# Performance work log

Measured on AMD Instinct MI355X. Metric: run time of the kernel, lower is better.

## Reference

```python
import jax, jax.numpy as jnp
import numpy as np

D = 512      # model dim
NH = 8       # heads
DH = 64      # dim per head
M = 256      # num landmarks
ITERS = 6    # pinv iterations
EPS = 1e-5   # layernorm eps


def layer_norm(x, g, b):
    mu = x.mean(-1, keepdims=True)
    var = ((x - mu) ** 2).mean(-1, keepdims=True)
    return (x - mu) * jax.lax.rsqrt(var + EPS) * g + b


def moore_penrose_pinv(x, iters=ITERS):
    abs_x = jnp.abs(x)
    col = abs_x.sum(-1)
    row = abs_x.sum(-2)
    z = jnp.swapaxes(x, -1, -2) / (jnp.max(col) * jnp.max(row))
    I = jnp.eye(x.shape[-1], dtype=x.dtype)
    for _ in range(iters):
        xz = x @ z
        z = 0.25 * z @ (13 * I - xz @ (15 * I - xz @ (7 * I - xz)))
    return z


def nystrom_attention(x, w_qkv, w_out, b_out, res_w):
    B, n0, _ = x.shape
    pad = (M - n0 % M) % M
    x = jnp.pad(x, ((0, 0), (pad, 0), (0, 0)))  # pad at front, like lucidrains
    n = n0 + pad
    qkv = x @ w_qkv  # (B, n, 3*D), no bias
    q, k, v = jnp.split(qkv, 3, axis=-1)
    rs = lambda t: t.reshape(B, n, NH, DH).transpose(0, 2, 1, 3)  # (B,H,n,d)
    q = rs(q) * (DH ** -0.5)
    k = rs(k)
    v = rs(v)
    l = n // M
    q_l = q.reshape(B, NH, M, l, DH).mean(3)  # (B,H,M,d) landmark means
    k_l = k.reshape(B, NH, M, l, DH).mean(3)
    s1 = jnp.einsum('bhnd,bhmd->bhnm', q, k_l)
    s2 = jnp.einsum('bhmd,bhld->bhml', q_l, k_l)
    s3 = jnp.einsum('bhmd,bhnd->bhmn', q_l, k)
    a1 = jax.nn.softmax(s1, -1)
    a2 = jax.nn.softmax(s2, -1)
    a3 = jax.nn.softmax(s3, -1)
    out = a1 @ (moore_penrose_pinv(a2) @ (a3 @ v))  # (B,H,n,d)
    # depthwise residual conv over sequence: Conv2d(heads, heads, (33,1), groups=heads)
    res = jax.lax.conv_general_dilated(v, res_w, (1, 1), 'SAME',
                                       feature_group_count=NH,
                                       dimension_numbers=('NCHW', 'OIHW', 'NCHW'))
    out = out + res
    out = out.transpose(0, 2, 1, 3).reshape(B, n, NH * DH) @ w_out + b_out
    return out[:, -n0:]


def dwconv(x, w, b):
    y = jax.lax.conv_general_dilated(x, w, (1, 1), 'SAME',
                                     feature_group_count=x.shape[1],
                                     dimension_numbers=('NCHW', 'OIHW', 'NCHW'))
    return y + b[None, :, None, None]


def ppeg(x, pw7, pb7, pw5, pb5, pw3, pb3, Hh, Ww):
    cls, feat = x[:, :1], x[:, 1:]
    B, _, C = x.shape
    cnn = feat.transpose(0, 2, 1).reshape(B, C, Hh, Ww)
    y = cnn + dwconv(cnn, pw7, pb7) + dwconv(cnn, pw5, pb5) + dwconv(cnn, pw3, pb3)
    y = y.reshape(B, C, Hh * Ww).transpose(0, 2, 1)
    return jnp.concatenate([cls, y], axis=1)


def _forward(x, w_fc1, b_fc1, cls_token, ln1_g, ln1_b, qkv1_w, out1_w, out1_b, res1_w,
             ln2_g, ln2_b, qkv2_w, out2_w, out2_b, res2_w,
             pw7, pb7, pw5, pb5, pw3, pb3, lnf_g, lnf_b, w_fc2, b_fc2):
    h = jax.nn.relu(x @ w_fc1 + b_fc1)  # (B, N, 512)
    Hn = h.shape[1]
    s = int(np.ceil(np.sqrt(Hn)))  # static grid side
    add = s * s - Hn
    h = jnp.concatenate([h, h[:, :add]], axis=1)
    B = h.shape[0]
    cls = jnp.broadcast_to(cls_token, (B, 1, D))
    h = jnp.concatenate([cls, h], axis=1)
    h = h + nystrom_attention(layer_norm(h, ln1_g, ln1_b), qkv1_w, out1_w, out1_b, res1_w)
    h = ppeg(h, pw7, pb7, pw5, pb5, pw3, pb3, s, s)
    h = h + nystrom_attention(layer_norm(h, ln2_g, ln2_b), qkv2_w, out2_w, out2_b, res2_w)
    h = layer_norm(h, lnf_g, lnf_b)[:, 0]
    return h @ w_fc2 + b_fc2


def setup_inputs() -> dict:
    key = jax.random.key(0)
    ks = jax.random.split(key, 16)
    g = lambda k, shp, s=0.02: jax.random.normal(k, shp, dtype=jnp.float32) * s
    z = lambda n: jnp.zeros((n,), jnp.float32)
    o = lambda n: jnp.ones((n,), jnp.float32)
    B, N, DIN, NC = 2, 10000, 1024, 2
    return {
        'x': jax.random.normal(ks[0], (B, N, DIN), dtype=jnp.float32),
        'w_fc1': g(ks[1], (DIN, D)), 'b_fc1': z(D),
        'cls_token': g(ks[2], (1, 1, D), 1.0),
        'ln1_g': o(D), 'ln1_b': z(D),
        'qkv1_w': g(ks[3], (D, 3 * D)),
        'out1_w': g(ks[4], (D, D)), 'out1_b': z(D),
        'res1_w': g(ks[5], (NH, 1, 33, 1)),
        'ln2_g': o(D), 'ln2_b': z(D),
        'qkv2_w': g(ks[6], (D, 3 * D)),
        'out2_w': g(ks[7], (D, D)), 'out2_b': z(D),
        'res2_w': g(ks[8], (NH, 1, 33, 1)),
        'pw7': g(ks[9], (D, 1, 7, 7)), 'pb7': z(D),
        'pw5': g(ks[10], (D, 1, 5, 5)), 'pb5': z(D),
        'pw3': g(ks[11], (D, 1, 3, 3)), 'pb3': z(D),
        'lnf_g': o(D), 'lnf_b': z(D),
        'w_fc2': g(ks[12], (D, NC)), 'b_fc2': z(NC),
    }


def reference(x, w_fc1, b_fc1, cls_token, ln1_g, ln1_b, qkv1_w, out1_w, out1_b, res1_w,
              ln2_g, ln2_b, qkv2_w, out2_w, out2_b, res2_w,
              pw7, pb7, pw5, pb5, pw3, pb3, lnf_g, lnf_b, w_fc2, b_fc2):
    logits = _forward(x, w_fc1, b_fc1, cls_token, ln1_g, ln1_b, qkv1_w, out1_w, out1_b, res1_w,
                      ln2_g, ln2_b, qkv2_w, out2_w, out2_b, res2_w,
                      pw7, pb7, pw5, pb5, pw3, pb3, lnf_g, lnf_b, w_fc2, b_fc2)
    Y_prob = jax.nn.softmax(logits, -1)
    Y_hat = jnp.argmax(logits, -1)
    return logits, Y_prob, Y_hat
```

## Files before the change

### kernel.cpp

```cpp
#include <hip/hip_runtime.h>
#include <math.h>

#define FLAG_RELU 1
#define FLAG_BIAS 2
#define FLAG_ACC  4
#define FLAG_ATOMIC 8

static constexpr int BB   = 2;
static constexpr int N0   = 10000;
static constexpr int DIN  = 1024;
static constexpr int D    = 512;
static constexpr int NH   = 8;
static constexpr int DH   = 64;
static constexpr int MM   = 256;
static constexpr int SEQ  = 10240;
static constexpr int PADR = 239;
static constexpr int NTOK = 10001;
static constexpr int LL   = 40;
static constexpr float EPS_ = 1e-5f;

typedef short short8v __attribute__((ext_vector_type(8)));
typedef float f32x4 __attribute__((ext_vector_type(4)));

__device__ __forceinline__ void atomicMaxPosF(float* addr, float v) {
    atomicMax((unsigned int*)addr, __float_as_uint(v));
}
__device__ __forceinline__ ushort f2bf(float f) {
    unsigned u = __float_as_uint(f);
    return (ushort)((u + 0x7FFFu + ((u >> 16) & 1u)) >> 16);
}
__device__ __forceinline__ float bf2f(ushort h) {
    return __uint_as_float(((unsigned)h) << 16);
}
__device__ __forceinline__ void split4(float4 f, ushort* ph, ushort* pl) {
    ushort4 hv, lv;
    hv.x = f2bf(f.x); lv.x = f2bf(f.x - bf2f(hv.x));
    hv.y = f2bf(f.y); lv.y = f2bf(f.y - bf2f(hv.y));
    hv.z = f2bf(f.z); lv.z = f2bf(f.z - bf2f(hv.z));
    hv.w = f2bf(f.w); lv.w = f2bf(f.w - bf2f(hv.w));
    *(ushort4*)ph = hv; *(ushort4*)pl = lv;
}
__device__ __forceinline__ void split8r(const float* p, short8v& h, short8v& l) {
    ushort hb[8], lb[8];
    split4(*(const float4*)p,     &hb[0], &lb[0]);
    split4(*(const float4*)(p+4), &hb[4], &lb[4]);
    h = *(short8v*)hb; l = *(short8v*)lb;
}

__global__ __launch_bounds__(256)
void mgemm128(const float* __restrict__ A, int lda, long long sAz,
              const ushort* __restrict__ BtH, const ushort* __restrict__ BtL, int ldbt,
              float* __restrict__ C, int ldc, long long sCz, const float* __restrict__ bias,
              int M, int N, int K, int flags, int qcols, float qscale)
{
    __shared__ ushort AsH[4*128*8], AsL[4*128*8], BsH[4*128*8], BsL[4*128*8];
    A += (size_t)blockIdx.z * sAz;
    C += (size_t)blockIdx.z * sCz;
    int t = threadIdx.x;
    int m0 = blockIdx.y * 128, n0 = blockIdx.x * 128;
    int w = t >> 6, lane = t & 63, q = lane >> 4, r = lane & 15;
    int wm = w >> 1, wn = w & 1;
    f32x4 acc[4][4];
    #pragma unroll
    for (int i = 0; i < 4; i++)
        #pragma unroll
        for (int j = 0; j < 4; j++) acc[i][j] = (f32x4){0.f,0.f,0.f,0.f};

    int srow = t >> 1, scg = (t & 1) * 16;
    int qg = (t & 1) * 2;
    int gm = m0 + srow;
    float4 pa0, pa1, pa2, pa3;
    uint4  pb0, pb1, pb2, pb3;
    {
        pa0 = pa1 = pa2 = pa3 = make_float4(0,0,0,0);
        if (gm < M) {
            const float* ap = A + (size_t)gm * lda + scg;
            pa0 = *(const float4*)(ap);   pa1 = *(const float4*)(ap+4);
            pa2 = *(const float4*)(ap+8); pa3 = *(const float4*)(ap+12);
        }
        size_t gb = (size_t)(n0 + srow) * ldbt + scg;
        pb0 = *(const uint4*)(BtH + gb); pb1 = *(const uint4*)(BtH + gb + 8);
        pb2 = *(const uint4*)(BtL + gb); pb3 = *(const uint4*)(BtL + gb + 8);
    }
    for (int k0 = 0; k0 < K; k0 += 32) {
        {
            ushort hb[16], lb[16];
            split4(pa0, &hb[0],  &lb[0]);
            split4(pa1, &hb[4],  &lb[4]);
            split4(pa2, &hb[8],  &lb[8]);
            split4(pa3, &hb[12], &lb[12]);
            *(uint4*)&AsH[(qg  )*1024 + srow*8] = *(uint4*)&hb[0];
            *(uint4*)&AsH[(qg+1)*1024 + srow*8] = *(uint4*)&hb[8];
            *(uint4*)&AsL[(qg  )*1024 + srow*8] = *(uint4*)&lb[0];
            *(uint4*)&AsL[(qg+1)*1024 + srow*8] = *(uint4*)&lb[8];
            *(uint4*)&BsH[(qg  )*1024 + srow*8] = pb0;
            *(uint4*)&BsH[(qg+1)*1024 + srow*8] = pb1;
            *(uint4*)&BsL[(qg  )*1024 + srow*8] = pb2;
            *(uint4*)&BsL[(qg+1)*1024 + srow*8] = pb3;
        }
        __syncthreads();
        if (k0 + 32 < K) {
            pa0 = pa1 = pa2 = pa3 = make_float4(0,0,0,0);
            if (gm < M) {
                const float* ap = A + (size_t)gm * lda + k0 + 32 + scg;
                pa0 = *(const float4*)(ap);   pa1 = *(const float4*)(ap+4);
                pa2 = *(const float4*)(ap+8); pa3 = *(const float4*)(ap+12);
            }
            size_t gb = (size_t)(n0 + srow) * ldbt + k0 + 32 + scg;
            pb0 = *(const uint4*)(BtH + gb); pb1 = *(const uint4*)(BtH + gb + 8);
            pb2 = *(const uint4*)(BtL + gb); pb3 = *(const uint4*)(BtL + gb + 8);
        }
        short8v ah[4], al[4];
        #pragma unroll
        for (int mi = 0; mi < 4; mi++) {
            int row = wm*64 + mi*16 + r;
            ah[mi] = *(const short8v*)&AsH[q*1024 + row*8];
            al[mi] = *(const short8v*)&AsL[q*1024 + row*8];
        }
        #pragma unroll
        for (int ni = 0; ni < 4; ni++) {
            int col = wn*64 + ni*16 + r;
            short8v bh = *(const short8v*)&BsH[q*1024 + col*8];
            short8v bl = *(const short8v*)&BsL[q*1024 + col*8];
            #pragma unroll
            for (int mi = 0; mi < 4; mi++) {
                acc[mi][ni] = __builtin_amdgcn_mfma_f32_16x16x32_bf16(ah[mi], bh, acc[mi][ni], 0,0,0);
                acc[mi][ni] = __builtin_amdgcn_mfma_f32_16x16x32_bf16(ah[mi], bl, acc[mi][ni], 0,0,0);
                acc[mi][ni] = __builtin_amdgcn_mfma_f32_16x16x32_bf16(al[mi], bh, acc[mi][ni], 0,0,0);
            }
        }
        __syncthreads();
    }
    #pragma unroll
    for (int mi = 0; mi < 4; mi++)
        #pragma unroll
        for (int ni = 0; ni < 4; ni++) {
            int gcol = n0 + wn*64 + ni*16 + r;
            float qs = (gcol < qcols) ? qscale : 1.f;
            float bv = (flags & FLAG_BIAS) ? bias[gcol] : 0.f;
            #pragma unroll
            for (int rg = 0; rg < 4; rg++) {
                int grow = m0 + wm*64 + mi*16 + q*4 + rg;
                if (grow >= M) continue;
                float v = acc[mi][ni][rg] * qs + bv;
                if (flags & FLAG_RELU) v = fmaxf(v, 0.f);
                float* cp = C + (size_t)grow * ldc + gcol;
                if (flags & FLAG_ACC) v += *cp;
                *cp = v;
            }
        }
}

__global__ __launch_bounds__(256)
void mbgemm64(const float* __restrict__ Abase, long long sAb, long long sAh, long long sAz, int lda,
              const ushort* __restrict__ BtH, const ushort* __restrict__ BtL,
              const float* __restrict__ Bnt, long long sBb, long long sBh, int ldb,
              float* __restrict__ Cbase, long long sCb, long long sCh, long long sCz, int ldc,
              ushort* __restrict__ eTH, ushort* __restrict__ eTL, long long sT, int ldct,
              int M, int N, int K, int nchunk,
              float dg, float bsc, float osc, int slab0, int flags)
{
    __shared__ ushort AsH[4*64*8], AsL[4*64*8], BsH[4*64*8], BsL[4*64*8];
    int zi = blockIdx.z / nchunk, ch = blockIdx.z % nchunk;
    int g = slab0 + zi, b = g >> 3, h = g & 7;
    const float* A = Abase + (size_t)b*sAb + (size_t)h*sAh + (size_t)zi*sAz;
    float* C = Cbase ? (Cbase + (size_t)b*sCb + (size_t)h*sCh + (size_t)zi*sCz) : nullptr;
    int kpc = K / nchunk;
    int kb = ch * kpc, ke = kb + kpc;
    int t = threadIdx.x;
    int m0 = blockIdx.y * 64, n0 = blockIdx.x * 64;
    int w = t >> 6, lane = t & 63, q = lane >> 4, r = lane & 15;
    int wm = w >> 1, wn = w & 1;
    f32x4 acc[2][2];
    #pragma unroll
    for (int i = 0; i < 2; i++)
        #pragma unroll
        for (int j = 0; j < 2; j++) acc[i][j] = (f32x4){0.f,0.f,0.f,0.f};

    int srow = t >> 2, scg = (t & 3) * 8;
    int qg = t & 3;
    const float* Abp = Bnt ? (Bnt + (size_t)b*sBb + (size_t)h*sBh) : nullptr;
    float4 pa0, pa1;
    float4 pf0, pf1;
    uint4  pu0, pu1;
    {
        const float* ap = A + (size_t)(m0 + srow) * lda + kb + scg;
        pa0 = *(const float4*)ap; pa1 = *(const float4*)(ap+4);
        if (Bnt) {
            const float* bp = Abp + (size_t)(n0 + srow) * ldb + kb + scg;
            pf0 = *(const float4*)bp; pf1 = *(const float4*)(bp+4);
        } else {
            size_t gb = (size_t)b*sBb + (size_t)h*sBh + (size_t)(n0 + srow) * ldb + kb + scg;
            pu0 = *(const uint4*)(BtH + gb); pu1 = *(const uint4*)(BtL + gb);
        }
    }
    for (int k0 = kb; k0 < ke; k0 += 32) {
        {
            ushort hb[8], lb[8];
            split4(pa0, &hb[0], &lb[0]);
            split4(pa1, &hb[4], &lb[4]);
            *(uint4*)&AsH[qg*512 + srow*8] = *(uint4*)&hb[0];
            *(uint4*)&AsL[qg*512 + srow*8] = *(uint4*)&lb[0];
            if (Bnt) {
                ushort hc[8], lc[8];
                split4(pf0, &hc[0], &lc[0]);
                split4(pf1, &hc[4], &lc[4]);
                *(uint4*)&BsH[qg*512 + srow*8] = *(uint4*)&hc[0];
                *(uint4*)&BsL[qg*512 + srow*8] = *(uint4*)&lc[0];
            } else {
                *(uint4*)&BsH[qg*512 + srow*8] = pu0;
                *(uint4*)&BsL[qg*512 + srow*8] = pu1;
            }
        }
        __syncthreads();
        if (k0 + 32 < ke) {
            const float* ap = A + (size_t)(m0 + srow) * lda + k0 + 32 + scg;
            pa0 = *(const float4*)ap; pa1 = *(const float4*)(ap+4);
            if (Bnt) {
                const float* bp = Abp + (size_t)(n0 + srow) * ldb + k0 + 32 + scg;
                pf0 = *(const float4*)bp; pf1 = *(const float4*)(bp+4);
            } else {
                size_t gb = (size_t)b*sBb + (size_t)h*sBh + (size_t)(n0 + srow) * ldb + k0 + 32 + scg;
                pu0 = *(const uint4*)(BtH + gb); pu1 = *(const uint4*)(BtL + gb);
            }
        }
        short8v ah[2], al[2];
        #pragma unroll
        for (int mi = 0; mi < 2; mi++) {
            int row = wm*32 + mi*16 + r;
            ah[mi] = *(const short8v*)&AsH[q*512 + row*8];
            al[mi] = *(const short8v*)&AsL[q*512 + row*8];
        }
        #pragma unroll
        for (int ni = 0; ni < 2; ni++) {
            int col = wn*32 + ni*16 + r;
            short8v bh = *(const short8v*)&BsH[q*512 + col*8];
            short8v bl = *(const short8v*)&BsL[q*512 + col*8];
            #pragma unroll
            for (int mi = 0; mi < 2; mi++) {
                acc[mi][ni] = __builtin_amdgcn_mfma_f32_16x16x32_bf16(ah[mi], bh, acc[mi][ni], 0,0,0);
                acc[mi][ni] = __builtin_amdgcn_mfma_f32_16x16x32_bf16(ah[mi], bl, acc[mi][ni], 0,0,0);
                acc[mi][ni] = __builtin_amdgcn_mfma_f32_16x16x32_bf16(al[mi], bh, acc[mi][ni], 0,0,0);
            }
        }
        __syncthreads();
    }
    bool dgnz = (dg != 0.f);
    #pragma unroll
    for (int mi = 0; mi < 2; mi++)
        #pragma unroll
        for (int ni = 0; ni < 2; ni++) {
            int gm0 = m0 + wm*32 + mi*16 + q*4;
            int gn  = n0 + wn*32 + ni*16 + r;
            float v[4];
            #pragma unroll
            for (int rg = 0; rg < 4; rg++) {
                float u = bsc * acc[mi][ni][rg];
                if (dgnz) u += dg * A[(size_t)(gm0+rg) * lda + gn];
                v[rg] = osc * u;
            }
            if (C) {
                if (flags & FLAG_ATOMIC) {
                    #pragma unroll
                    for (int rg = 0; rg < 4; rg++)
                        atomicAdd(C + (size_t)(gm0+rg) * ldc + gn, v[rg]);
                } else {
                    #pragma unroll
                    for (int rg = 0; rg < 4; rg++)
                        C[(size_t)(gm0+rg) * ldc + gn] = v[rg];
                }
            }
            if (eTH) {
                ushort4 hv, lv;
                hv.x = f2bf(v[0]); lv.x = f2bf(v[0] - bf2f(hv.x));
                hv.y = f2bf(v[1]); lv.y = f2bf(v[1] - bf2f(hv.y));
                hv.z = f2bf(v[2]); lv.z = f2bf(v[2] - bf2f(hv.z));
                hv.w = f2bf(v[3]); lv.w = f2bf(v[3] - bf2f(hv.w));
                size_t to = (size_t)g * sT + (size_t)gn * ldct + gm0;
                *(ushort4*)(eTH + to) = hv;
                *(ushort4*)(eTL + to) = lv;
            }
        }
}

__global__ __launch_bounds__(256)
void a1_fused(const float* __restrict__ qkv,
              const ushort* __restrict__ klH, const ushort* __restrict__ klL,
              const ushort* __restrict__ wbH, const ushort* __restrict__ wbL,
              float* __restrict__ attn)
{
    __shared__ float Pc[256*66];
    __shared__ float redm[4][64];
    __shared__ float reds[4][64];
    int g = blockIdx.y, b = g >> 3, h = g & 7;
    int tok0 = blockIdx.x * 64;
    int t = threadIdx.x;
    int w = t >> 6, lane = t & 63, q = lane >> 4, r = lane & 15;

    f32x4 acc[4][4];
    #pragma unroll
    for (int i = 0; i < 4; i++)
        #pragma unroll
        for (int j = 0; j < 4; j++) acc[i][j] = (f32x4){0.f,0.f,0.f,0.f};
    #pragma unroll
    for (int k0 = 0; k0 < 64; k0 += 32) {
        short8v ah[4], al[4];
        #pragma unroll
        for (int mi = 0; mi < 4; mi++) {
            const float* ap = qkv + ((size_t)b*SEQ + tok0 + mi*16 + r) * 1536
                            + h*DH + k0 + q*8;
            split8r(ap, ah[mi], al[mi]);
        }
        #pragma unroll
        for (int ni = 0; ni < 4; ni++) {
            size_t kb = ((size_t)g*MM + w*64 + ni*16 + r) * DH + k0 + q*8;
            short8v bh = *(const short8v*)(klH + kb);
            short8v bl = *(const short8v*)(klL + kb);
            #pragma unroll
            for (int mi = 0; mi < 4; mi++) {
                acc[mi][ni] = __builtin_amdgcn_mfma_f32_16x16x32_bf16(ah[mi], bh, acc[mi][ni], 0,0,0);
                acc[mi][ni] = __builtin_amdgcn_mfma_f32_16x16x32_bf16(ah[mi], bl, acc[mi][ni], 0,0,0);
                acc[mi][ni] = __builtin_amdgcn_mfma_f32_16x16x32_bf16(al[mi], bh, acc[mi][ni], 0,0,0);
            }
        }
    }
    #pragma unroll
    for (int mi = 0; mi < 4; mi++)
        #pragma unroll
        for (int rg = 0; rg < 4; rg++) {
            float m = fmaxf(fmaxf(acc[mi][0][rg], acc[mi][1][rg]),
                            fmaxf(acc[mi][2][rg], acc[mi][3][rg]));
            for (int o = 8; o > 0; o >>= 1) m = fmaxf(m, __shfl_xor(m, o));
            if (r == 0) redm[w][mi*16 + q*4 + rg] = m;
        }
    __syncthreads();
    #pragma unroll
    for (int mi = 0; mi < 4; mi++)
        #pragma unroll
        for (int rg = 0; rg < 4; rg++) {
            int row = mi*16 + q*4 + rg;
            float gm = fmaxf(fmaxf(redm[0][row], redm[1][row]),
                             fmaxf(redm[2][row], redm[3][row]));
            float s = 0.f;
            #pragma unroll
            for (int ni = 0; ni < 4; ni++) {
                float e = expf(acc[mi][ni][rg] - gm);
                acc[mi][ni][rg] = e;
                s += e;
            }
            for (int o = 8; o > 0; o >>= 1) s += __shfl_xor(s, o);
            if (r == 0) reds[w][row] = s;
        }
    #pragma unroll
    for (int mi = 0; mi < 4; mi++)
        #pragma unroll
        for (int ni = 0; ni < 4; ni++) {
            int col = w*64 + ni*16 + r;
            int row0 = mi*16 + q*4;
            float* pp = &Pc[col*66 + row0];
            *(float2*)(pp)     = make_float2(acc[mi][ni][0], acc[mi][ni][1]);
            *(float2*)(pp + 2) = make_float2(acc[mi][ni][2], acc[mi][ni][3]);
        }
    __syncthreads();
    f32x4 oacc[4];
    #pragma unroll
    for (int ni = 0; ni < 4; ni++) oacc[ni] = (f32x4){0.f,0.f,0.f,0.f};
    for (int k0 = 0; k0 < 8; k0++) {
        short8v ph, pl;
        {
            ushort hb[8], lb[8];
            #pragma unroll
            for (int j = 0; j < 8; j++) {
                int k = k0*32 + q*8 + j;
                float p = Pc[k*66 + w*16 + r];
                hb[j] = f2bf(p); lb[j] = f2bf(p - bf2f(hb[j]));
            }
            ph = *(short8v*)hb; pl = *(short8v*)lb;
        }
        #pragma unroll
        for (int ni = 0; ni < 4; ni++) {
            size_t wo = ((size_t)g*64 + ni*16 + r) * MM + k0*32 + q*8;
            short8v bh = *(const short8v*)(wbH + wo);
            short8v bl = *(const short8v*)(wbL + wo);
            oacc[ni] = __builtin_amdgcn_mfma_f32_16x16x32_bf16(ph, bh, oacc[ni], 0,0,0);
            oacc[ni] = __builtin_amdgcn_mfma_f32_16x16x32_bf16(ph, bl, oacc[ni], 0,0,0);
            oacc[ni] = __builtin_amdgcn_mfma_f32_16x16x32_bf16(pl, bh, oacc[ni], 0,0,0);
        }
    }
    float inv[4];
    #pragma unroll
    for (int rg = 0; rg < 4; rg++) {
        int row = w*16 + q*4 + rg;
        inv[rg] = 1.0f / (reds[0][row] + reds[1][row] + reds[2][row] + reds[3][row]);
    }
    #pragma unroll
    for (int ni = 0; ni < 4; ni++)
        #pragma unroll
        for (int rg = 0; rg < 4; rg++) {
            int tok = tok0 + w*16 + q*4 + rg;
            attn[((size_t)b*SEQ + tok) * D + h*DH + ni*16 + r] = oacc[ni][rg] * inv[rg];
        }
}

__global__ __launch_bounds__(256)
void convsplitT(const float* __restrict__ in, ushort* __restrict__ oh, ushort* __restrict__ ol,
                int R, int C, int ldin, long long sInB, long long sInH, long long sInZ,
                int ldo, long long sOutZ)
{
    __shared__ float tile[32][33];
    int z = blockIdx.z, b = z >> 3, h = z & 7;
    const float* I = in + (size_t)b*sInB + (size_t)h*sInH + (size_t)z*sInZ;
    int p0 = blockIdx.x * 32, c0 = blockIdx.y * 32;
    int tx = threadIdx.x & 31, ty = threadIdx.x >> 5;
    #pragma unroll
    for (int k = 0; k < 4; k++) {
        int rr = p0 + ty + k*8, cc = c0 + tx;
        tile[ty + k*8][tx] = (rr < R && cc < C) ? I[(size_t)rr * ldin + cc] : 0.f;
    }
    __syncthreads();
    #pragma unroll
    for (int k = 0; k < 4; k++) {
        int rr = p0 + tx, cc = c0 + ty + k*8;
        if (rr < R && cc < C) {
            float f = tile[tx][ty + k*8];
            ushort hv = f2bf(f);
            size_t o = (size_t)z * sOutZ + (size_t)cc * ldo + rr;
            oh[o] = hv; ol[o] = f2bf(f - bf2f(hv));
        }
    }
}

__global__ void fill_cls(const float* __restrict__ cls, float* __restrict__ H) {
    H[(size_t)blockIdx.x * NTOK * D + threadIdx.x] = cls[threadIdx.x];
}

__global__ __launch_bounds__(256)
void ln_pad(const float* __restrict__ H, const float* __restrict__ g,
            const float* __restrict__ bt, float* __restrict__ out)
{
    int blk = blockIdx.x;
    int b = blk / SEQ, i = blk % SEQ;
    int t = threadIdx.x;
    float* orow = out + (size_t)blk * D;
    if (i < PADR) { orow[t] = 0.f; orow[t+256] = 0.f; return; }
    const float* x = H + ((size_t)b * NTOK + (i - PADR)) * D;
    float v0 = x[t], v1 = x[t+256];
    __shared__ float w1[4], w2[4];
    float s = v0 + v1;
    for (int o = 32; o > 0; o >>= 1) s += __shfl_xor(s, o);
    if ((t & 63) == 0) w1[t >> 6] = s;
    __syncthreads();
    float mu = (w1[0]+w1[1]+w1[2]+w1[3]) * (1.0f / D);
    float d0 = v0 - mu, d1 = v1 - mu;
    float qq = d0*d0 + d1*d1;
    for (int o = 32; o > 0; o >>= 1) qq += __shfl_xor(qq, o);
    if ((t & 63) == 0) w2[t >> 6] = qq;
    __syncthreads();
    float rs = rsqrtf((w2[0]+w2[1]+w2[2]+w2[3]) * (1.0f / D) + EPS_);
    orow[t]     = d0 * rs * g[t]     + bt[t];
    orow[t+256] = d1 * rs * g[t+256] + bt[t+256];
}

__global__ __launch_bounds__(512)
void landmarks(const float* __restrict__ qkv, float* __restrict__ ql,
               float* __restrict__ klt, ushort* __restrict__ klH, ushort* __restrict__ klL)
{
    int blk = blockIdx.x;
    int b = blk >> 8, m = blk & 255;
    int c = threadIdx.x;
    const float* base = qkv + ((size_t)b * SEQ + (size_t)m * LL) * 1536;
    float sq0=0,sq1=0,sq2=0,sq3=0, sk0=0,sk1=0,sk2=0,sk3=0;
    for (int tt = 0; tt < LL; tt += 4) {
        const float* rr = base + (size_t)tt * 1536;
        sq0 += rr[c];          sk0 += rr[512 + c];
        sq1 += rr[1536 + c];   sk1 += rr[1536 + 512 + c];
        sq2 += rr[3072 + c];   sk2 += rr[3072 + 512 + c];
        sq3 += rr[4608 + c];   sk3 += rr[4608 + 512 + c];
    }
    float sq = (sq0+sq1+sq2+sq3) * (1.0f / LL);
    float sk = (sk0+sk1+sk2+sk3) * (1.0f / LL);
    int h = c >> 6, d = c & 63;
    int slab = b * NH + h;
    ql [((size_t)slab * MM + m) * DH + d] = sq;
    klt[((size_t)slab * DH + d) * MM + m] = sk;
    size_t kidx = ((size_t)slab * MM + m) * DH + d;
    ushort kh = f2bf(sk);
    klH[kidx] = kh; klL[kidx] = f2bf(sk - bf2f(kh));
}

__global__ __launch_bounds__(256)
void s2_softmax(const float* __restrict__ ql, const float* __restrict__ klt,
                float* __restrict__ a2)
{
    int blk = blockIdx.x;
    int m = blk & 255, slab = blk >> 8;
    int j = threadIdx.x;
    __shared__ float q[64];
    __shared__ float red[256];
    if (j < 64) q[j] = ql[((size_t)slab * MM + m) * DH + j];
    __syncthreads();
    const float* kt = klt + (size_t)slab * DH * MM;
    float s = 0.f;
    #pragma unroll 8
    for (int kk = 0; kk < 64; kk++) s = fmaf(q[kk], kt[kk*MM + j], s);
    red[j] = s; __syncthreads();
    for (int o = 128; o > 0; o >>= 1) { if (j < o) red[j] = fmaxf(red[j], red[j+o]); __syncthreads(); }
    float mx = red[0]; __syncthreads();
    float e = expf(s - mx);
    red[j] = e; __syncthreads();
    for (int o = 128; o > 0; o >>= 1) { if (j < o) red[j] += red[j+o]; __syncthreads(); }
    a2[((size_t)slab * MM + m) * MM + j] = e / red[0];
}

__global__ void zero_scr(float* s) { if (threadIdx.x < 2) s[threadIdx.x] = 0.f; }

__global__ __launch_bounds__(256)
void a2_alpha(const float* __restrict__ a2, float* __restrict__ scr)
{
    int slab = blockIdx.x, t = threadIdx.x;
    const float* A = a2 + (size_t)slab * MM * MM;
    float cs = 0.f, rs = 0.f;
    for (int rr = 0; rr < MM; rr++) cs += fabsf(A[(size_t)rr * MM + t]);
    for (int cc = 0; cc < MM; cc++) rs += fabsf(A[(size_t)t * MM + cc]);
    __shared__ float red[256];
    red[t] = rs; __syncthreads();
    for (int o = 128; o > 0; o >>= 1) { if (t < o) red[t] = fmaxf(red[t], red[t+o]); __syncthreads(); }
    float mrs = red[0]; __syncthreads();
    red[t] = cs; __syncthreads();
    for (int o = 128; o > 0; o >>= 1) { if (t < o) red[t] = fmaxf(red[t], red[t+o]); __syncthreads(); }
    float mcs = red[0];
    if (t == 0) { atomicMaxPosF(scr + 0, mrs); atomicMaxPosF(scr + 1, mcs); }
}

__global__ __launch_bounds__(256)
void z_init(const float* __restrict__ a2, const float* __restrict__ scr,
            float* __restrict__ z, ushort* __restrict__ zTh, ushort* __restrict__ zTl)
{
    size_t idx = (size_t)blockIdx.x * 256 + threadIdx.x;
    int slab = (int)(idx >> 16), rr = (int)((idx >> 8) & 255), cc = (int)(idx & 255);
    float inv = 1.0f / (scr[0] * scr[1]);
    z[idx] = a2[((size_t)slab << 16) + (size_t)cc * MM + rr] * inv;
    float tv = a2[idx] * inv;
    ushort th = f2bf(tv);
    zTh[idx] = th; zTl[idx] = f2bf(tv - bf2f(th));
}

__global__ __launch_bounds__(256)
void s3_softmax(float* __restrict__ s3)
{
    float* row = s3 + (size_t)blockIdx.x * SEQ;
    int t = threadIdx.x;
    float4 v[10];
    #pragma unroll
    for (int i = 0; i < 10; i++) v[i] = *(const float4*)(row + 4*(i*256 + t));
    float mx = -3.4e38f;
    #pragma unroll
    for (int i = 0; i < 10; i++)
        mx = fmaxf(mx, fmaxf(fmaxf(v[i].x, v[i].y), fmaxf(v[i].z, v[i].w)));
    __shared__ float red[4];
    for (int o = 32; o > 0; o >>= 1) mx = fmaxf(mx, __shfl_xor(mx, o));
    if ((t & 63) == 0) red[t >> 6] = mx;
    __syncthreads();
    mx = fmaxf(fmaxf(red[0], red[1]), fmaxf(red[2], red[3]));
    float sum = 0.f;
    #pragma unroll
    for (int i = 0; i < 10; i++) {
        v[i].x = expf(v[i].x - mx); v[i].y = expf(v[i].y - mx);
        v[i].z = expf(v[i].z - mx); v[i].w = expf(v[i].w - mx);
        sum += v[i].x + v[i].y + v[i].z + v[i].w;
    }
    __shared__ float red2[4];
    for (int o = 32; o > 0; o >>= 1) sum += __shfl_xor(sum, o);
    if ((t & 63) == 0) red2[t >> 6] = sum;
    __syncthreads();
    float inv = 1.0f / (red2[0] + red2[1] + red2[2] + red2[3]);
    #pragma unroll
    for (int i = 0; i < 10; i++) {
        v[i].x *= inv; v[i].y *= inv; v[i].z *= inv; v[i].w *= inv;
        *(float4*)(row + 4*(i*256 + t)) = v[i];
    }
}

__global__ __launch_bounds__(512)
void res_add(const float* __restrict__ qkv, const float* __restrict__ rw,
             float* __restrict__ attn)
{
    int blk = blockIdx.x;
    int b = blk / (SEQ/16), i0 = (blk % (SEQ/16)) * 16;
    int c = threadIdx.x, h = c >> 6;
    __shared__ float w[NH*33];
    if (c < NH*33) w[c] = rw[c];
    __syncthreads();
    float acc[16];
    float* ab = attn + ((size_t)b * SEQ + i0) * D + c;
    #pragma unroll
    for (int rr = 0; rr < 16; rr++) acc[rr] = ab[(size_t)rr * D];
    const float* vb = qkv + (size_t)b * SEQ * 1536 + 2*D + c;
    const float* wh = w + h * 33;
    #pragma unroll 4
    for (int jj = 0; jj < 48; jj++) {
        int j = i0 + jj - 16;
        float val = ((unsigned)j < (unsigned)SEQ) ? vb[(size_t)j * 1536] : 0.f;
        #pragma unroll
        for (int rr = 0; rr < 16; rr++) {
            int ky = jj - rr;
            if (ky >= 0 && ky < 33) acc[rr] = fmaf(val, wh[ky], acc[rr]);
        }
    }
    #pragma unroll
    for (int rr = 0; rr < 16; rr++) ab[(size_t)rr * D] = acc[rr];
}

__global__ __launch_bounds__(256)
void t_fw(const float* __restrict__ H, float* __restrict__ P)
{
    __shared__ float tile[32][33];
    int p0 = blockIdx.x * 32, c0 = blockIdx.y * 32, b = blockIdx.z;
    int tx = threadIdx.x & 31, ty = threadIdx.x >> 5;
    #pragma unroll
    for (int k = 0; k < 4; k++) {
        int pos = p0 + ty + k*8;
        tile[ty + k*8][tx] = (pos < 10000)
            ? H[((size_t)b * NTOK + 1 + pos) * D + c0 + tx] : 0.f;
    }
    __syncthreads();
    #pragma unroll
    for (int k = 0; k < 4; k++) {
        int c = c0 + ty + k*8, pos = p0 + tx;
        if (pos < 10000)
            P[((size_t)b * D + c) * 10000 + pos] = tile[tx][ty + k*8];
    }
}

__global__ __launch_bounds__(256)
void ppeg_conv(const float* __restrict__ P,
               const float* __restrict__ w7, const float* __restrict__ b7,
               const float* __restrict__ w5, const float* __restrict__ b5,
               const float* __restrict__ w3, const float* __restrict__ b3,
               float* __restrict__ Q)
{
    __shared__ float PS[106 * 107];
    __shared__ float w7s[49], w5s[25], w3s[9];
    int blk = blockIdx.x;
    int b = blk >> 9, c = blk & 511;
    int t = threadIdx.x;
    for (int idx = t; idx < 106*107; idx += 256) PS[idx] = 0.f;
    if (t < 49) w7s[t] = w7[(size_t)c * 49 + t];
    if (t < 25) w5s[t] = w5[(size_t)c * 25 + t];
    if (t < 9)  w3s[t] = w3[(size_t)c * 9 + t];
    float bsum = b7[c] + b5[c] + b3[c];
    __syncthreads();
    const float* Pin = P + ((size_t)b * D + c) * 10000;
    for (int p = t; p < 10000; p += 256) {
        int y = p / 100, x = p - y * 100;
        PS[(y + 3) * 107 + x + 3] = Pin[p];
    }
    __syncthreads();
    float* Qo = Q + ((size_t)b * D + c) * 10000;
    for (int task = t; task < 2500; task += 256) {
        int ry = task / 100, x = task - ry * 100;
        int y0 = ry * 4;
        float a0 = bsum + PS[(y0+3)*107 + x+3];
        float a1 = bsum + PS[(y0+4)*107 + x+3];
        float a2 = bsum + PS[(y0+5)*107 + x+3];
        float a3 = bsum + PS[(y0+6)*107 + x+3];
        #pragma unroll
        for (int rr = 0; rr < 10; rr++) {
            const float* rp = &PS[(y0 + rr) * 107 + x];
            #pragma unroll
            for (int kx = 0; kx < 7; kx++) {
                float v = rp[kx];
                if (rr < 7)            a0 = fmaf(v, w7s[rr*7 + kx], a0);
                if (rr >= 1 && rr < 8) a1 = fmaf(v, w7s[(rr-1)*7 + kx], a1);
                if (rr >= 2 && rr < 9) a2 = fmaf(v, w7s[(rr-2)*7 + kx], a2);
                if (rr >= 3)           a3 = fmaf(v, w7s[(rr-3)*7 + kx], a3);
            }
        }
        #pragma unroll
        for (int rr = 0; rr < 8; rr++) {
            const float* rp = &PS[(y0 + rr + 1) * 107 + x + 1];
            #pragma unroll
            for (int kx = 0; kx < 5; kx++) {
                float v = rp[kx];
                if (rr < 5)            a0 = fmaf(v, w5s[rr*5 + kx], a0);
                if (rr >= 1 && rr < 6) a1 = fmaf(v, w5s[(rr-1)*5 + kx], a1);
                if (rr >= 2 && rr < 7) a2 = fmaf(v, w5s[(rr-2)*5 + kx], a2);
                if (rr >= 3)           a3 = fmaf(v, w5s[(rr-3)*5 + kx], a3);
            }
        }
        #pragma unroll
        for (int rr = 0; rr < 6; rr++) {
            const float* rp = &PS[(y0 + rr + 2) * 107 + x + 2];
            #pragma unroll
            for (int kx = 0; kx < 3; kx++) {
                float v = rp[kx];
                if (rr < 3)            a0 = fmaf(v, w3s[rr*3 + kx], a0);
                if (rr >= 1 && rr < 4) a1 = fmaf(v, w3s[(rr-1)*3 + kx], a1);
                if (rr >= 2 && rr < 5) a2 = fmaf(v, w3s[(rr-2)*3 + kx], a2);
                if (rr >= 3)           a3 = fmaf(v, w3s[(rr-3)*3 + kx], a3);
            }
        }
        Qo[(y0+0)*100 + x] = a0;
        Qo[(y0+1)*100 + x] = a1;
        Qo[(y0+2)*100 + x] = a2;
        Qo[(y0+3)*100 + x] = a3;
    }
}

__global__ __launch_bounds__(256)
void t_bw(const float* __restrict__ Q, float* __restrict__ H)
{
    __shared__ float tile[32][33];
    int p0 = blockIdx.x * 32, c0 = blockIdx.y * 32, b = blockIdx.z;
    int tx = threadIdx.x & 31, ty = threadIdx.x >> 5;
    #pragma unroll
    for (int k = 0; k < 4; k++) {
        int c = c0 + ty + k*8, pos = p0 + tx;
        tile[ty + k*8][tx] = (pos < 10000)
            ? Q[((size_t)b * D + c) * 10000 + pos] : 0.f;
    }
    __syncthreads();
    #pragma unroll
    for (int k = 0; k < 4; k++) {
        int pos = p0 + ty + k*8;
        if (pos < 10000)
            H[((size_t)b * NTOK + 1 + pos) * D + c0 + tx] = tile[tx][ty + k*8];
    }
}

__global__ __launch_bounds__(512)
void final_head(const float* __restrict__ H, const float* __restrict__ g,
                const float* __restrict__ bt, const float* __restrict__ w2,
                const float* __restrict__ b2, float* __restrict__ out)
{
    int b = blockIdx.x, t = threadIdx.x;
    __shared__ float red[512];
    float v = H[(size_t)b * NTOK * D + t];
    red[t] = v; __syncthreads();
    for (int o = 256; o > 0; o >>= 1) { if (t < o) red[t] += red[t+o]; __syncthreads(); }
    float mu = red[0] * (1.0f / D); __syncthreads();
    float dv = v - mu;
    red[t] = dv*dv; __syncthreads();
    for (int o = 256; o > 0; o >>= 1) { if (t < o) red[t] += red[t+o]; __syncthreads(); }
    float rstd = rsqrtf(red[0] * (1.0f / D) + EPS_); __syncthreads();
    float xn = dv * rstd * g[t] + bt[t];
    red[t] = xn * w2[2*t]; __syncthreads();
    for (int o = 256; o > 0; o >>= 1) { if (t < o) red[t] += red[t+o]; __syncthreads(); }
    float l0 = red[0] + b2[0]; __syncthreads();
    red[t] = xn * w2[2*t+1]; __syncthreads();
    for (int o = 256; o > 0; o >>= 1) { if (t < o) red[t] += red[t+o]; __syncthreads(); }
    float l1 = red[0] + b2[1];
    if (t == 0) {
        out[b*2+0] = l0; out[b*2+1] = l1;
        float mx = fmaxf(l0, l1);
        float e0 = expf(l0 - mx), e1 = expf(l1 - mx);
        float ssum = e0 + e1;
        out[4 + b*2 + 0] = e0 / ssum;
        out[4 + b*2 + 1] = e1 / ssum;
        out[8 + b] = (l1 > l0) ? 1.0f : 0.0f;
    }
}

extern "C" void kernel_launch(void* const* d_in, const int* in_sizes, int n_in,
                              void* d_out, int out_size, void* d_ws, size_t ws_size,
                              hipStream_t stream)
{
    const float* x      = (const float*)d_in[0];
    const float* w_fc1  = (const float*)d_in[1];
    const float* b_fc1  = (const float*)d_in[2];
    const float* cls    = (const float*)d_in[3];
    const float* ln1_g  = (const float*)d_in[4];
    const float* ln1_b  = (const float*)d_in[5];
    const float* qkv1_w = (const float*)d_in[6];
    const float* out1_w = (const float*)d_in[7];
    const float* out1_b = (const float*)d_in[8];
    const float* res1_w = (const float*)d_in[9];
    const float* ln2_g  = (const float*)d_in[10];
    const float* ln2_b  = (const float*)d_in[11];
    const float* qkv2_w = (const float*)d_in[12];
    const float* out2_w = (const float*)d_in[13];
    const float* out2_b = (const float*)d_in[14];
    const float* res2_w = (const float*)d_in[15];
    const float* pw7 = (const float*)d_in[16];
    const float* pb7 = (const float*)d_in[17];
    const float* pw5 = (const float*)d_in[18];
    const float* pb5 = (const float*)d_in[19];
    const float* pw3 = (const float*)d_in[20];
    const float* pb3 = (const float*)d_in[21];
    const float* lnf_g = (const float*)d_in[22];
    const float* lnf_b = (const float*)d_in[23];
    const float* w_fc2 = (const float*)d_in[24];
    const float* b_fc2 = (const float*)d_in[25];

    float* ws = (float*)d_ws;
    size_t off = 0;
    auto alloc = [&](size_t n) { float* p = ws + off; off += (n + 63) & ~(size_t)63; return p; };
    float* H    = alloc((size_t)BB * NTOK * D);
    float* LN   = alloc((size_t)BB * SEQ * D);
    float* QKV  = alloc((size_t)BB * SEQ * 3 * D);
    float* QL   = alloc((size_t)BB * NH * MM * DH);
    float* KLT  = alloc((size_t)BB * NH * DH * MM);
    float* A2   = alloc((size_t)BB * NH * MM * MM);
    float* ZA   = alloc((size_t)BB * NH * MM * MM);
    float* ZB   = alloc((size_t)BB * NH * MM * MM);
    float* XZ   = alloc((size_t)BB * NH * MM * MM);
    float* A3V  = alloc((size_t)BB * NH * MM * DH);
    float* WB   = alloc((size_t)BB * NH * MM * DH);
    float* S3   = alloc((size_t)8 * MM * SEQ);
    float* SCR  = alloc(64);
    auto ualloc = [&](size_t n) { ushort* p = (ushort*)(ws + off); off += ((n + 127) / 2) & ~(size_t)63; return p; };
    ushort* WTfcH = ualloc((size_t)512 * 1024);
    ushort* WTfcL = ualloc((size_t)512 * 1024);
    ushort* WTqH  = ualloc((size_t)1536 * 512);
    ushort* WTqL  = ualloc((size_t)1536 * 512);
    ushort* WToH  = ualloc((size_t)512 * 512);
    ushort* WToL  = ualloc((size_t)512 * 512);
    ushort* klBH  = ualloc((size_t)16 * MM * DH);
    ushort* klBL  = ualloc((size_t)16 * MM * DH);
    float*  ATTN = LN;
    ushort* VTH  = (ushort*)LN;
    ushort* VTL  = VTH + (size_t)16 * DH * SEQ;
    ushort* A3VTH = (ushort*)ZB;
    ushort* A3VTL = A3VTH + (size_t)16 * DH * MM;
    ushort* WBTH  = A3VTL + (size_t)16 * DH * MM;
    ushort* WBTL  = WBTH  + (size_t)16 * DH * MM;
    ushort* PT   = (ushort*)S3;
    const size_t PS_ = (size_t)16 * 65536;
    ushort* zTAH = PT;            ushort* zTAL = PT + PS_;
    ushort* zTBH = PT + 2*PS_;    ushort* zTBL = PT + 3*PS_;
    ushort* XZTH = PT + 4*PS_;    ushort* XZTL = PT + 5*PS_;
    ushort* T1TH = PT + 6*PS_;    ushort* T1TL = PT + 7*PS_;
    ushort* T2TH = PT + 8*PS_;    ushort* T2TL = PT + 9*PS_;
    (void)ws_size; (void)in_sizes; (void)n_in; (void)out_size;

    convsplitT<<<dim3(32,16,1), 256, 0, stream>>>(w_fc1, WTfcH, WTfcL, 1024, 512, 512, 0,0,0, 1024, 0);
    mgemm128<<<dim3(4, 79, BB), 256, 0, stream>>>(x, DIN, (long long)N0*DIN,
        WTfcH, WTfcL, 1024, H + D, D, (long long)NTOK*D, b_fc1,
        N0, D, DIN, FLAG_BIAS|FLAG_RELU, 0, 1.f);
    fill_cls<<<BB, D, 0, stream>>>(cls, H);

    auto attention = [&](const float* lg, const float* lb,
                         const float* qw, const float* ow,
                         const float* ob, const float* rw)
    {
        convsplitT<<<dim3(16,48,1), 256, 0, stream>>>(qw, WTqH, WTqL, 512, 1536, 1536, 0,0,0, 512, 0);
        convsplitT<<<dim3(16,16,1), 256, 0, stream>>>(ow, WToH, WToL, 512, 512, 512, 0,0,0, 512, 0);
        ln_pad<<<BB*SEQ, 256, 0, stream>>>(H, lg, lb, LN);
        mgemm128<<<dim3(12, 160, 1), 256, 0, stream>>>(LN, D, 0, WTqH, WTqL, D,
            QKV, 3*D, 0, nullptr, BB*SEQ, 3*D, D, 0, D, 0.125f);
        convsplitT<<<dim3(320, 2, 16), 256, 0, stream>>>(QKV + 2*D, VTH, VTL,
            SEQ, DH, 1536, (long long)SEQ*1536, 64, 0, SEQ, (long long)DH*SEQ);
        landmarks<<<BB*MM, 512, 0, stream>>>(QKV, QL, KLT, klBH, klBL);
        s2_softmax<<<BB*NH*MM, 256, 0, stream>>>(QL, KLT, A2);
        zero_scr<<<1, 64, 0, stream>>>(SCR);
        a2_alpha<<<BB*NH, 256, 0, stream>>>(A2, SCR);
        z_init<<<BB*NH*MM*MM/256, 256, 0, stream>>>(A2, SCR, ZA, zTAH, zTAL);
        float* z = ZA; float* zn = ZB;
        ushort *zTcH = zTAH, *zTcL = zTAL, *zTnH = zTBH, *zTnL = zTBL;
        for (int it = 0; it < 6; it++) {
            dim3 g(4, 4, 16);
            mbgemm64<<<g,256,0,stream>>>(A2, 0,0,65536LL, MM,
                zTcH, zTcL, nullptr, 8LL*65536, 65536LL, MM,
                XZ, 0,0,65536LL, MM, XZTH, XZTL, 65536LL, MM,
                MM, MM, MM, 1, 0.f, 1.f, 1.f, 0, 0);
            mbgemm64<<<g,256,0,stream>>>(XZ, 0,0,65536LL, MM,
                XZTH, XZTL, nullptr, 8LL*65536, 65536LL, MM,
                nullptr, 0,0,0, MM, T1TH, T1TL, 65536LL, MM,
                MM, MM, MM, 1, 7.f, -1.f, 1.f, 0, 0);
            mbgemm64<<<g,256,0,stream>>>(XZ, 0,0,65536LL, MM,
                T1TH, T1TL, nullptr, 8LL*65536, 65536LL, MM,
                nullptr, 0,0,0, MM, T2TH, T2TL, 65536LL, MM,
                MM, MM, MM, 1, 15.f, -1.f, 1.f, 0, 0);
            mbgemm64<<<g,256,0,stream>>>(z, 0,0,65536LL, MM,
                T2TH, T2TL, nullptr, 8LL*65536, 65536LL, MM,
                zn, 0,0,65536LL, MM, zTnH, zTnL, 65536LL, MM,
                MM, MM, MM, 1, 13.f, -1.f, 0.25f, 0, 0);
            float* ts = z; z = zn; zn = ts;
            ushort* uh = zTcH; zTcH = zTnH; zTnH = uh;
            ushort* ul = zTcL; zTcL = zTnL; zTnL = ul;
        }
        for (int grp = 0; grp < 2; grp++) {
            int slab0 = grp * 8;
            mbgemm64<<<dim3(160, 4, 8), 256, 0, stream>>>(QL, 8LL*16384, 16384LL, 0, DH,
                nullptr, nullptr, QKV + D, (long long)SEQ*1536, 64LL, 1536,
                S3, 0,0,(long long)MM*SEQ, SEQ, nullptr, nullptr, 0, 0,
                MM, SEQ, DH, 1, 0.f, 1.f, 1.f, slab0, 0);
            s3_softmax<<<8*MM, 256, 0, stream>>>(S3);
            hipMemsetAsync(A3V + (size_t)slab0 * MM * DH, 0,
                           (size_t)8 * MM * DH * sizeof(float), stream);
            mbgemm64<<<dim3(1, 4, 8*16), 256, 0, stream>>>(S3, 0,0,(long long)MM*SEQ, SEQ,
                VTH, VTL, nullptr, 8LL*DH*SEQ, (long long)DH*SEQ, SEQ,
                A3V, 8LL*16384, 16384LL, 0, DH, nullptr, nullptr, 0, 0,
                MM, DH, SEQ, 16, 0.f, 1.f, 1.f, slab0, FLAG_ATOMIC);
        }
        convsplitT<<<dim3(8, 2, 16), 256, 0, stream>>>(A3V, A3VTH, A3VTL,
            MM, DH, DH, 0, 0, 16384LL, MM, 16384LL);
        mbgemm64<<<dim3(1, 4, 16), 256, 0, stream>>>(z, 0,0,65536LL, MM,
            A3VTH, A3VTL, nullptr, 8LL*16384, 16384LL, MM,
            WB, 8LL*16384, 16384LL, 0, DH, WBTH, WBTL, 16384LL, MM,
            MM, DH, MM, 1, 0.f, 1.f, 1.f, 0, 0);
        a1_fused<<<dim3(SEQ/64, 16), 256, 0, stream>>>(QKV, klBH, klBL, WBTH, WBTL, ATTN);
        res_add<<<BB*SEQ/16, 512, 0, stream>>>(QKV, rw, ATTN);
        mgemm128<<<dim3(4, 79, BB), 256, 0, stream>>>(ATTN + (size_t)PADR*D, D, (long long)SEQ*D,
            WToH, WToL, D, H, D, (long long)NTOK*D, ob,
            NTOK, D, D, FLAG_BIAS|FLAG_ACC, 0, 1.f);
    };

    attention(ln1_g, ln1_b, qkv1_w, out1_w, out1_b, res1_w);

    {
        float* Pp = S3;
        float* Qp = S3 + (size_t)BB * D * 10000;
        dim3 tg((10000 + 31)/32, D/32, BB);
        t_fw<<<tg, 256, 0, stream>>>(H, Pp);
        ppeg_conv<<<BB*D, 256, 0, stream>>>(Pp, pw7, pb7, pw5, pb5, pw3, pb3, Qp);
        t_bw<<<tg, 256, 0, stream>>>(Qp, H);
    }

    attention(ln2_g, ln2_b, qkv2_w, out2_w, out2_b, res2_w);

    final_head<<<BB, 512, 0, stream>>>(H, lnf_g, lnf_b, w_fc2, b_fc2, (float*)d_out);
}
```

Before: 2.372 ms.

## Fuse s3 softmax normalization into A3·V GEMM load and shrink a1 tile

The s3 softmax kernel now computes only the per-row max and inverse sum. The exp and normalization are applied inside mbgemm64 when it loads the A operand, which removes a full write of the normalized S3 buffer. Separately, a1_fused drops to 32 tokens per block, doubling the grid and cutting shared-memory use to raise occupancy. In exchange, the GEMM recomputes exp in its load path, and the smaller a1 tile means more reloads of landmark keys and weights.

```diff
diff --git a/kernel.cpp b/kernel.cpp
--- a/kernel.cpp
+++ b/kernel.cpp
@@ -157,6 +157,7 @@
               const float* __restrict__ Bnt, long long sBb, long long sBh, int ldb,
               float* __restrict__ Cbase, long long sCb, long long sCh, long long sCz, int ldc,
               ushort* __restrict__ eTH, ushort* __restrict__ eTL, long long sT, int ldct,
+              const float* __restrict__ rowM, const float* __restrict__ rowI,
               int M, int N, int K, int nchunk,
               float dg, float bsc, float osc, int slab0, int flags)
 {
@@ -179,6 +180,12 @@
 
     int srow = t >> 2, scg = (t & 3) * 8;
     int qg = t & 3;
+    float rmv = 0.f, riv = 1.f;
+    bool doexp = (rowM != nullptr);
+    if (doexp) {
+        rmv = rowM[(size_t)zi * MM + m0 + srow];
+        riv = rowI[(size_t)zi * MM + m0 + srow];
+    }
     const float* Abp = Bnt ? (Bnt + (size_t)b*sBb + (size_t)h*sBh) : nullptr;
     float4 pa0, pa1;
     float4 pf0, pf1;
@@ -196,9 +203,16 @@
     }
     for (int k0 = kb; k0 < ke; k0 += 32) {
         {
+            float4 qa0 = pa0, qa1 = pa1;
+            if (doexp) {
+                qa0.x = expf(qa0.x - rmv) * riv; qa0.y = expf(qa0.y - rmv) * riv;
+                qa0.z = expf(qa0.z - rmv) * riv; qa0.w = expf(qa0.w - rmv) * riv;
+                qa1.x = expf(qa1.x - rmv) * riv; qa1.y = expf(qa1.y - rmv) * riv;
+                qa1.z = expf(qa1.z - rmv) * riv; qa1.w = expf(qa1.w - rmv) * riv;
+            }
             ushort hb[8], lb[8];
-            split4(pa0, &hb[0], &lb[0]);
-            split4(pa1, &hb[4], &lb[4]);
+            split4(qa0, &hb[0], &lb[0]);
+            split4(qa1, &hb[4], &lb[4]);
             *(uint4*)&AsH[qg*512 + srow*8] = *(uint4*)&hb[0];
             *(uint4*)&AsL[qg*512 + srow*8] = *(uint4*)&lb[0];
             if (Bnt) {
@@ -289,24 +303,24 @@
               const ushort* __restrict__ wbH, const ushort* __restrict__ wbL,
               float* __restrict__ attn)
 {
-    __shared__ float Pc[256*66];
-    __shared__ float redm[4][64];
-    __shared__ float reds[4][64];
+    __shared__ float Pc[256*35];
+    __shared__ float redm[4][32];
+    __shared__ float reds[4][32];
     int g = blockIdx.y, b = g >> 3, h = g & 7;
-    int tok0 = blockIdx.x * 64;
+    int tok0 = blockIdx.x * 32;
     int t = threadIdx.x;
     int w = t >> 6, lane = t & 63, q = lane >> 4, r = lane & 15;
 
-    f32x4 acc[4][4];
-    #pragma unroll
-    for (int i = 0; i < 4; i++)
+    f32x4 acc[2][4];
+    #pragma unroll
+    for (int i = 0; i < 2; i++)
         #pragma unroll
         for (int j = 0; j < 4; j++) acc[i][j] = (f32x4){0.f,0.f,0.f,0.f};
     #pragma unroll
     for (int k0 = 0; k0 < 64; k0 += 32) {
-        short8v ah[4], al[4];
-        #pragma unroll
-        for (int mi = 0; mi < 4; mi++) {
+        short8v ah[2], al[2];
+        #pragma unroll
+        for (int mi = 0; mi < 2; mi++) {
             const float* ap = qkv + ((size_t)b*SEQ + tok0 + mi*16 + r) * 1536
                             + h*DH + k0 + q*8;
             split8r(ap, ah[mi], al[mi]);
@@ -317,7 +331,7 @@
             short8v bh = *(const short8v*)(klH + kb);
             short8v bl = *(const short8v*)(klL + kb);
             #pragma unroll
-            for (int mi = 0; mi < 4; mi++) {
+            for (int mi = 0; mi < 2; mi++) {
                 acc[mi][ni] = __builtin_amdgcn_mfma_f32_16x16x32_bf16(ah[mi], bh, acc[mi][ni], 0,0,0);
                 acc[mi][ni] = __builtin_amdgcn_mfma_f32_16x16x32_bf16(ah[mi], bl, acc[mi][ni], 0,0,0);
                 acc[mi][ni] = __builtin_amdgcn_mfma_f32_16x16x32_bf16(al[mi], bh, acc[mi][ni], 0,0,0);
@@ -325,7 +339,7 @@
         }
     }
     #pragma unroll
-    for (int mi = 0; mi < 4; mi++)
+    for (int mi = 0; mi < 2; mi++)
         #pragma unroll
         for (int rg = 0; rg < 4; rg++) {
             float m = fmaxf(fmaxf(acc[mi][0][rg], acc[mi][1][rg]),
@@ -335,7 +349,7 @@
         }
     __syncthreads();
     #pragma unroll
-    for (int mi = 0; mi < 4; mi++)
+    for (int mi = 0; mi < 2; mi++)
         #pragma unroll
         for (int rg = 0; rg < 4; rg++) {
             int row = mi*16 + q*4 + rg;
@@ -352,19 +366,20 @@
             if (r == 0) reds[w][row] = s;
         }
     #pragma unroll
-    for (int mi = 0; mi < 4; mi++)
+    for (int mi = 0; mi < 2; mi++)
         #pragma unroll
         for (int ni = 0; ni < 4; ni++) {
             int col = w*64 + ni*16 + r;
             int row0 = mi*16 + q*4;
-            float* pp = &Pc[col*66 + row0];
+            float* pp = &Pc[col*35 + row0];
             *(float2*)(pp)     = make_float2(acc[mi][ni][0], acc[mi][ni][1]);
             *(float2*)(pp + 2) = make_float2(acc[mi][ni][2], acc[mi][ni][3]);
         }
     __syncthreads();
-    f32x4 oacc[4];
-    #pragma unroll
-    for (int ni = 0; ni < 4; ni++) oacc[ni] = (f32x4){0.f,0.f,0.f,0.f};
+    int wm = w & 1, wn = w >> 1;
+    f32x4 oacc[2];
+    #pragma unroll
+    for (int ni = 0; ni < 2; ni++) oacc[ni] = (f32x4){0.f,0.f,0.f,0.f};
     for (int k0 = 0; k0 < 8; k0++) {
         short8v ph, pl;
         {
@@ -372,14 +387,14 @@
             #pragma unroll
             for (int j = 0; j < 8; j++) {
                 int k = k0*32 + q*8 + j;
-                float p = Pc[k*66 + w*16 + r];
+                float p = Pc[k*35 + wm*16 + r];
                 hb[j] = f2bf(p); lb[j] = f2bf(p - bf2f(hb[j]));
             }
             ph = *(short8v*)hb; pl = *(short8v*)lb;
         }
         #pragma unroll
-        for (int ni = 0; ni < 4; ni++) {
-            size_t wo = ((size_t)g*64 + ni*16 + r) * MM + k0*32 + q*8;
+        for (int ni = 0; ni < 2; ni++) {
+            size_t wo = ((size_t)g*64 + wn*32 + ni*16 + r) * MM + k0*32 + q*8;
             short8v bh = *(const short8v*)(wbH + wo);
             short8v bl = *(const short8v*)(wbL + wo);
             oacc[ni] = __builtin_amdgcn_mfma_f32_16x16x32_bf16(ph, bh, oacc[ni], 0,0,0);
@@ -390,15 +405,15 @@
     float inv[4];
     #pragma unroll
     for (int rg = 0; rg < 4; rg++) {
-        int row = w*16 + q*4 + rg;
+        int row = wm*16 + q*4 + rg;
         inv[rg] = 1.0f / (reds[0][row] + reds[1][row] + reds[2][row] + reds[3][row]);
     }
     #pragma unroll
-    for (int ni = 0; ni < 4; ni++)
+    for (int ni = 0; ni < 2; ni++)
         #pragma unroll
         for (int rg = 0; rg < 4; rg++) {
-            int tok = tok0 + w*16 + q*4 + rg;
-            attn[((size_t)b*SEQ + tok) * D + h*DH + ni*16 + r] = oacc[ni][rg] * inv[rg];
+            int tok = tok0 + wm*16 + q*4 + rg;
+            attn[((size_t)b*SEQ + tok) * D + h*DH + wn*32 + ni*16 + r] = oacc[ni][rg] * inv[rg];
         }
 }
 
@@ -546,9 +561,10 @@
 }
 
 __global__ __launch_bounds__(256)
-void s3_softmax(float* __restrict__ s3)
-{
-    float* row = s3 + (size_t)blockIdx.x * SEQ;
+void s3_maxsum(const float* __restrict__ s3, float* __restrict__ rowM,
+               float* __restrict__ rowI)
+{
+    const float* row = s3 + (size_t)blockIdx.x * SEQ;
     int t = threadIdx.x;
     float4 v[10];
     #pragma unroll
@@ -565,19 +581,16 @@
     float sum = 0.f;
     #pragma unroll
     for (int i = 0; i < 10; i++) {
-        v[i].x = expf(v[i].x - mx); v[i].y = expf(v[i].y - mx);
-        v[i].z = expf(v[i].z - mx); v[i].w = expf(v[i].w - mx);
-        sum += v[i].x + v[i].y + v[i].z + v[i].w;
+        sum += expf(v[i].x - mx) + expf(v[i].y - mx)
+             + expf(v[i].z - mx) + expf(v[i].w - mx);
     }
     __shared__ float red2[4];
     for (int o = 32; o > 0; o >>= 1) sum += __shfl_xor(sum, o);
     if ((t & 63) == 0) red2[t >> 6] = sum;
     __syncthreads();
-    float inv = 1.0f / (red2[0] + red2[1] + red2[2] + red2[3]);
-    #pragma unroll
-    for (int i = 0; i < 10; i++) {
-        v[i].x *= inv; v[i].y *= inv; v[i].z *= inv; v[i].w *= inv;
-        *(float4*)(row + 4*(i*256 + t)) = v[i];
+    if (t == 0) {
+        rowM[blockIdx.x] = mx;
+        rowI[blockIdx.x] = 1.0f / (red2[0] + red2[1] + red2[2] + red2[3]);
     }
 }
 
@@ -808,6 +821,8 @@
     float* WB   = alloc((size_t)BB * NH * MM * DH);
     float* S3   = alloc((size_t)8 * MM * SEQ);
     float* SCR  = alloc(64);
+    float* ROWM = alloc((size_t)8 * MM);
+    float* ROWI = alloc((size_t)8 * MM);
     auto ualloc = [&](size_t n) { ushort* p = (ushort*)(ws + off); off += ((n + 127) / 2) & ~(size_t)63; return p; };
     ushort* WTfcH = ualloc((size_t)512 * 1024);
     ushort* WTfcL = ualloc((size_t)512 * 1024);
@@ -862,18 +877,22 @@
             mbgemm64<<<g,256,0,stream>>>(A2, 0,0,65536LL, MM,
                 zTcH, zTcL, nullptr, 8LL*65536, 65536LL, MM,
                 XZ, 0,0,65536LL, MM, XZTH, XZTL, 65536LL, MM,
+                nullptr, nullptr,
                 MM, MM, MM, 1, 0.f, 1.f, 1.f, 0, 0);
             mbgemm64<<<g,256,0,stream>>>(XZ, 0,0,65536LL, MM,
                 XZTH, XZTL, nullptr, 8LL*65536, 65536LL, MM,
                 nullptr, 0,0,0, MM, T1TH, T1TL, 65536LL, MM,
+                nullptr, nullptr,
                 MM, MM, MM, 1, 7.f, -1.f, 1.f, 0, 0);
             mbgemm64<<<g,256,0,stream>>>(XZ, 0,0,65536LL, MM,
                 T1TH, T1TL, nullptr, 8LL*65536, 65536LL, MM,
                 nullptr, 0,0,0, MM, T2TH, T2TL, 65536LL, MM,
+                nullptr, nullptr,
                 MM, MM, MM, 1, 15.f, -1.f, 1.f, 0, 0);
             mbgemm64<<<g,256,0,stream>>>(z, 0,0,65536LL, MM,
                 T2TH, T2TL, nullptr, 8LL*65536, 65536LL, MM,
                 zn, 0,0,65536LL, MM, zTnH, zTnL, 65536LL, MM,
+                nullptr, nullptr,
                 MM, MM, MM, 1, 13.f, -1.f, 0.25f, 0, 0);
             float* ts = z; z = zn; zn = ts;
             ushort* uh = zTcH; zTcH = zTnH; zTnH = uh;
@@ -884,13 +903,15 @@
             mbgemm64<<<dim3(160, 4, 8), 256, 0, stream>>>(QL, 8LL*16384, 16384LL, 0, DH,
                 nullptr, nullptr, QKV + D, (long long)SEQ*1536, 64LL, 1536,
                 S3, 0,0,(long long)MM*SEQ, SEQ, nullptr, nullptr, 0, 0,
+                nullptr, nullptr,
                 MM, SEQ, DH, 1, 0.f, 1.f, 1.f, slab0, 0);
-            s3_softmax<<<8*MM, 256, 0, stream>>>(S3);
+            s3_maxsum<<<8*MM, 256, 0, stream>>>(S3, ROWM, ROWI);
             hipMemsetAsync(A3V + (size_t)slab0 * MM * DH, 0,
                            (size_t)8 * MM * DH * sizeof(float), stream);
             mbgemm64<<<dim3(1, 4, 8*16), 256, 0, stream>>>(S3, 0,0,(long long)MM*SEQ, SEQ,
                 VTH, VTL, nullptr, 8LL*DH*SEQ, (long long)DH*SEQ, SEQ,
                 A3V, 8LL*16384, 16384LL, 0, DH, nullptr, nullptr, 0, 0,
+                ROWM, ROWI,
                 MM, DH, SEQ, 16, 0.f, 1.f, 1.f, slab0, FLAG_ATOMIC);
         }
         convsplitT<<<dim3(8, 2, 16), 256, 0, stream>>>(A3V, A3VTH, A3VTL,
@@ -898,8 +919,9 @@
         mbgemm64<<<dim3(1, 4, 16), 256, 0, stream>>>(z, 0,0,65536LL, MM,
             A3VTH, A3VTL, nullptr, 8LL*16384, 16384LL, MM,
             WB, 8LL*16384, 16384LL, 0, DH, WBTH, WBTL, 16384LL, MM,
+            nullptr, nullptr,
             MM, DH, MM, 1, 0.f, 1.f, 1.f, 0, 0);
-        a1_fused<<<dim3(SEQ/64, 16), 256, 0, stream>>>(QKV, klBH, klBL, WBTH, WBTL, ATTN);
+        a1_fused<<<dim3(SEQ/32, 16), 256, 0, stream>>>(QKV, klBH, klBL, WBTH, WBTL, ATTN);
         res_add<<<BB*SEQ/16, 512, 0, stream>>>(QKV, rw, ATTN);
         mgemm128<<<dim3(4, 79, BB), 256, 0, stream>>>(ATTN + (size_t)PADR*D, D, (long long)SEQ*D,
             WToH, WToL, D, H, D, (long long)NTOK*D, ob,
```

Result: no change. 2.407 ms (+1.5%).
